# Optimization experiments

Hardware: AMD Instinct MI355X
Metric: run time of the kernel (lower is better)

## Reference

```python
import jax, jax.numpy as jnp
import numpy as np

EPS = 1e-6
NUM_HEADS = 16

def _favor_positive_features(x):
    # softmax-style normalized positive features along last dim
    p = jnp.exp(x - jnp.max(x, axis=-1, keepdims=True))
    return p / (jnp.sum(p, axis=-1, keepdims=True) + EPS)

def setup_inputs() -> dict:
    key = jax.random.key(0)
    ks = jax.random.split(key, 9)
    B, L, D = 2, 2048, 1024
    s = 0.02
    return {
        "hidden_states": jax.random.normal(ks[0], (B, L, D), dtype=jnp.float32),
        # Linear weights stored as [in, out] (y = x @ W + b), matching torch Linear math
        "Wq": jax.random.normal(ks[1], (D, D), dtype=jnp.float32) * s,
        "bq": jnp.zeros((D,), dtype=jnp.float32),
        "Wk": jax.random.normal(ks[2], (D, D), dtype=jnp.float32) * s,
        "bk": jnp.zeros((D,), dtype=jnp.float32),
        "Wv": jax.random.normal(ks[3], (D, D), dtype=jnp.float32) * s,
        "bv": jnp.zeros((D,), dtype=jnp.float32),
        "Wo": jax.random.normal(ks[4], (D, D), dtype=jnp.float32) * s,
        "bo": jnp.zeros((D,), dtype=jnp.float32),
    }

def reference(hidden_states, Wq, bq, Wk, bk, Wv, bv, Wo, bo):
    B, L, D = hidden_states.shape
    H = NUM_HEADS
    hd = D // H

    def split_heads(x):  # [B,L,D] -> [B,H,L,hd]
        return x.reshape(B, L, H, hd).transpose(0, 2, 1, 3)

    q = split_heads(hidden_states @ Wq + bq)
    k = split_heads(hidden_states @ Wk + bk)
    v = split_heads(hidden_states @ Wv + bv)

    q = _favor_positive_features(q)
    k = _favor_positive_features(k)

    # quadratic scores as in the original module
    numerator = jnp.einsum('bhld,bhmd->bhlm', q, k)
    # einsum(q, ones) over d == sum_d q, broadcast over m (identical math)
    denominator = jnp.sum(q, axis=-1, keepdims=True)  # [B,H,L,1]
    attention_probs = numerator / (denominator + EPS)
    # dropout prob = 0.0 -> identity
    context = jnp.einsum('bhlm,bhmd->bhld', attention_probs, v)
    context = context.transpose(0, 2, 1, 3).reshape(B, L, D)
    return context @ Wo + bo
```

## Files before the change

kernel.cpp:

```cpp
#include <hip/hip_runtime.h>


#define EPSV 1e-6f
#define MDIM 4096
#define DDIM 1024
#define HEADS 16
#define HD 64

typedef __attribute__((ext_vector_type(8))) _Float16 half8;
typedef __attribute__((ext_vector_type(4))) _Float16 half4;
typedef __attribute__((ext_vector_type(4))) float f32x4;

__device__ inline void gld_lds16(const _Float16* g, _Float16* l) {
    __builtin_amdgcn_global_load_lds(
        (const __attribute__((address_space(1))) unsigned int*)g,
        (__attribute__((address_space(3))) unsigned int*)l, 16, 0, 0);
}

__global__ __launch_bounds__(256) void xhalf_kernel(const float* __restrict__ x,
                                                    _Float16* __restrict__ xh)
{
    const int i = (blockIdx.x * 256 + threadIdx.x) * 8;
    const float4 v0 = *(const float4*)&x[i];
    const float4 v1 = *(const float4*)&x[i + 4];
    half8 h;
    h[0] = (_Float16)v0.x; h[1] = (_Float16)v0.y; h[2] = (_Float16)v0.z; h[3] = (_Float16)v0.w;
    h[4] = (_Float16)v1.x; h[5] = (_Float16)v1.y; h[6] = (_Float16)v1.z; h[7] = (_Float16)v1.w;
    *(half8*)&xh[i] = h;
}

__global__ __launch_bounds__(256) void wsplit_kernel(
    const float* __restrict__ W0, const float* __restrict__ W1,
    const float* __restrict__ W2, const float* __restrict__ W3,
    _Float16* __restrict__ T0h, _Float16* __restrict__ T0l,
    _Float16* __restrict__ T1h, _Float16* __restrict__ T1l,
    _Float16* __restrict__ T2h, _Float16* __restrict__ T2l,
    _Float16* __restrict__ T3h, _Float16* __restrict__ T3l)
{
    const float* W; _Float16* Th; _Float16* Tl;
    if (blockIdx.z == 0)      { W = W0; Th = T0h; Tl = T0l; }
    else if (blockIdx.z == 1) { W = W1; Th = T1h; Tl = T1l; }
    else if (blockIdx.z == 2) { W = W2; Th = T2h; Tl = T2l; }
    else                      { W = W3; Th = T3h; Tl = T3l; }

    __shared__ float t[32][33];
    const int tt = threadIdx.x;
    const int r = tt >> 3, c4 = (tt & 7) * 4;
    const int k0 = blockIdx.x * 32, n0 = blockIdx.y * 32;

    const float4 v = *(const float4*)&W[(size_t)(k0 + r) * DDIM + n0 + c4];
    t[r][c4 + 0] = v.x; t[r][c4 + 1] = v.y; t[r][c4 + 2] = v.z; t[r][c4 + 3] = v.w;
    __syncthreads();

    const float x0 = t[c4 + 0][r], x1 = t[c4 + 1][r], x2 = t[c4 + 2][r], x3 = t[c4 + 3][r];
    half4 h, l;
    h[0] = (_Float16)x0; l[0] = (_Float16)((x0 - (float)h[0]) * 256.0f);
    h[1] = (_Float16)x1; l[1] = (_Float16)((x1 - (float)h[1]) * 256.0f);
    h[2] = (_Float16)x2; l[2] = (_Float16)((x2 - (float)h[2]) * 256.0f);
    h[3] = (_Float16)x3; l[3] = (_Float16)((x3 - (float)h[3]) * 256.0f);
    *(half4*)&Th[(size_t)(n0 + r) * DDIM + k0 + c4] = h;
    *(half4*)&Tl[(size_t)(n0 + r) * DDIM + k0 + c4] = l;
}

template<int WJ>
__global__ __launch_bounds__(256, 2) void gemm_mfma(
    const _Float16* __restrict__ A,
    const _Float16* __restrict__ B0h, const _Float16* __restrict__ B0l,
    const _Float16* __restrict__ B1h, const _Float16* __restrict__ B1l,
    const _Float16* __restrict__ B2h, const _Float16* __restrict__ B2l,
    const float* __restrict__ bias0, const float* __restrict__ bias1, const float* __restrict__ bias2,
    float* __restrict__ C0, float* __restrict__ C1, float* __restrict__ C2)
{
    const _Float16* Bh; const _Float16* Bl; const float* bias; float* C;
    if (blockIdx.z == 0)      { Bh = B0h; Bl = B0l; bias = bias0; C = C0; }
    else if (blockIdx.z == 1) { Bh = B1h; Bl = B1l; bias = bias1; C = C1; }
    else                      { Bh = B2h; Bl = B2l; bias = bias2; C = C2; }

    constexpr int FA = 8;
    constexpr int FB = 2 * WJ;
    constexpr int NF = FA + 2 * FB;
    constexpr int FPW = NF / 4;
    constexpr int NT = DDIM / 32;

    __shared__ __align__(16) _Float16 lds[2][NF * 512];

    const int tid = threadIdx.x;
    const int w = tid >> 6, l = tid & 63;
    const int row0 = blockIdx.x * 128, col0 = blockIdx.y * (32 * WJ);
    const int wr = w >> 1, wc = w & 1;

    const int lrow = (l & 15);
    const int lk   = (l >> 4) * 8;

    const _Float16* gsrc[FPW];
    #pragma unroll
    for (int u = 0; u < FPW; ++u) {
        const int g = w * FPW + u;
        const _Float16* src; int outer;
        if (g < FA)           { src = A;  outer = row0 + g * 16; }
        else if (g < FA + FB) { src = Bh; outer = col0 + (g - FA) * 16; }
        else                  { src = Bl; outer = col0 + (g - FA - FB) * 16; }
        gsrc[u] = src + (size_t)(outer + lrow) * DDIM + lk;
    }

    f32x4 acc1[4][WJ], acc2[4][WJ];
    #pragma unroll
    for (int i = 0; i < 4; ++i)
        #pragma unroll
        for (int j = 0; j < WJ; ++j) {
            acc1[i][j] = (f32x4){0.f, 0.f, 0.f, 0.f};
            acc2[i][j] = (f32x4){0.f, 0.f, 0.f, 0.f};
        }

    #pragma unroll
    for (int u = 0; u < FPW; ++u)
        gld_lds16(gsrc[u], &lds[0][(w * FPW + u) * 512]);
    __syncthreads();

    int cur = 0;
    for (int t = 0; t < NT; ++t) {
        if (t + 1 < NT) {
            const int kc = (t + 1) * 32;
            #pragma unroll
            for (int u = 0; u < FPW; ++u)
                gld_lds16(gsrc[u] + kc, &lds[cur ^ 1][(w * FPW + u) * 512]);
        }

        const _Float16* lbase = &lds[cur][0];
        half8 a[4], bh[WJ], bl[WJ];
        #pragma unroll
        for (int i = 0; i < 4; ++i)
            a[i] = *(const half8*)&lbase[(wr * 4 + i) * 512 + l * 8];
        #pragma unroll
        for (int j = 0; j < WJ; ++j) {
            bh[j] = *(const half8*)&lbase[(FA + wc * WJ + j) * 512 + l * 8];
            bl[j] = *(const half8*)&lbase[(FA + FB + wc * WJ + j) * 512 + l * 8];
        }
        #pragma unroll
        for (int i = 0; i < 4; ++i)
            #pragma unroll
            for (int j = 0; j < WJ; ++j) {
                acc1[i][j] = __builtin_amdgcn_mfma_f32_16x16x32_f16(a[i], bh[j], acc1[i][j], 0, 0, 0);
                acc2[i][j] = __builtin_amdgcn_mfma_f32_16x16x32_f16(a[i], bl[j], acc2[i][j], 0, 0, 0);
            }

        __syncthreads();
        cur ^= 1;
    }

    #pragma unroll
    for (int j = 0; j < WJ; ++j) {
        const int col = col0 + (wc * WJ + j) * 16 + lrow;
        const float bb = bias[col];
        #pragma unroll
        for (int i = 0; i < 4; ++i) {
            const int rbase = row0 + (wr * 4 + i) * 16 + (l >> 4) * 4;
            #pragma unroll
            for (int q = 0; q < 4; ++q)
                C[(size_t)(rbase + q) * DDIM + col] =
                    acc1[i][j][q] + acc2[i][j][q] * 0.00390625f + bb;
        }
    }
}

__global__ __launch_bounds__(256) void feature_kernel(float* __restrict__ buf,
                                                      float* __restrict__ den)
{
    const int wid  = blockIdx.x * 4 + (threadIdx.x >> 6);
    const int lane = threadIdx.x & 63;
    const int row = wid >> 4;
    const int h   = wid & 15;
    float* p = buf + (size_t)row * DDIM + h * HD;

    const float v = p[lane];
    float m = v;
    #pragma unroll
    for (int o = 32; o; o >>= 1) m = fmaxf(m, __shfl_xor(m, o, 64));
    const float e = expf(v - m);
    float s = e;
    #pragma unroll
    for (int o = 32; o; o >>= 1) s += __shfl_xor(s, o, 64);
    const float q = e / (s + EPSV);
    p[lane] = q;
    if (den != nullptr) {
        float d = q;
        #pragma unroll
        for (int o = 32; o; o >>= 1) d += __shfl_xor(d, o, 64);
        if (lane == 0) den[wid] = d;
    }
}

#define MSUB 32
__global__ __launch_bounds__(256) void kv_partial_kernel(
    const float* __restrict__ Kf, const float* __restrict__ V, float* __restrict__ KVp)
{
    const int z = blockIdx.x;
    const int chunk = z & 7;
    const int bh = z >> 3;
    const int h = bh & 15;
    const int b = bh >> 4;

    __shared__ float Ks[MSUB][HD];
    __shared__ float Vs[MSUB][HD];

    const int t = threadIdx.x;
    const int d0 = (t >> 4) * 4;
    const int e0 = (t & 15) * 4;
    float acc[4][4];
    #pragma unroll
    for (int i = 0; i < 4; ++i)
        #pragma unroll
        for (int j = 0; j < 4; ++j) acc[i][j] = 0.f;

    const int base_tok = b * 2048 + chunk * 256;
    for (int sc = 0; sc < 8; ++sc) {
        __syncthreads();
        #pragma unroll
        for (int u = 0; u < 2; ++u) {
            const int f = t + u * 256;
            const int tok = f >> 4;
            const int c4 = (f & 15) * 4;
            const size_t g = (size_t)(base_tok + sc * MSUB + tok) * DDIM + h * HD + c4;
            *(float4*)&Ks[tok][c4] = *(const float4*)&Kf[g];
            *(float4*)&Vs[tok][c4] = *(const float4*)&V[g];
        }
        __syncthreads();
        #pragma unroll
        for (int mm = 0; mm < MSUB; ++mm) {
            const float4 k4 = *(const float4*)&Ks[mm][d0];
            const float4 v4 = *(const float4*)&Vs[mm][e0];
            const float kr[4] = {k4.x, k4.y, k4.z, k4.w};
            const float vr[4] = {v4.x, v4.y, v4.z, v4.w};
            #pragma unroll
            for (int i = 0; i < 4; ++i)
                #pragma unroll
                for (int j = 0; j < 4; ++j)
                    acc[i][j] = fmaf(kr[i], vr[j], acc[i][j]);
        }
    }
    float* outp = KVp + (size_t)z * 4096;
    #pragma unroll
    for (int i = 0; i < 4; ++i)
        *(float4*)&outp[(d0 + i) * HD + e0] =
            make_float4(acc[i][0], acc[i][1], acc[i][2], acc[i][3]);
}

__global__ __launch_bounds__(256) void kv_reduce_kernel(const float* __restrict__ KVp,
                                                        float* __restrict__ KV)
{
    const int idx = blockIdx.x * 256 + threadIdx.x;
    const int bh = idx >> 12;
    const int off = idx & 4095;
    float s = 0.f;
    #pragma unroll
    for (int c = 0; c < 8; ++c) s += KVp[(size_t)(bh * 8 + c) * 4096 + off];
    KV[idx] = s;
}

__global__ __launch_bounds__(256) void context_kernel(
    const float* __restrict__ QF, const float* __restrict__ KV, const float* __restrict__ den,
    _Float16* __restrict__ Ch)
{
    const int z = blockIdx.x;
    const int tc = z & 31;
    const int bh = z >> 5;
    const int h = bh & 15;
    const int b = bh >> 4;

    __shared__ float KVs[HD][HD];
    const int t = threadIdx.x;
    #pragma unroll
    for (int u = 0; u < 4; ++u) {
        const int f = t + u * 256;
        *(float4*)&KVs[0][f * 4] = *(const float4*)&KV[(size_t)bh * 4096 + f * 4];
    }
    __syncthreads();

    const int wave = t >> 6;
    const int lane = t & 63;
    for (int it = 0; it < 16; ++it) {
        const int tok = tc * 64 + it * 4 + wave;
        const int row = b * 2048 + tok;
        const size_t idx = (size_t)row * DDIM + h * HD + lane;
        const float qv = QF[idx];
        float acc = 0.f;
        #pragma unroll
        for (int e = 0; e < 64; ++e) {
            const float qe = __shfl(qv, e, 64);
            acc = fmaf(qe, KVs[e][lane], acc);
        }
        const float r = acc / (den[row * HEADS + h] + EPSV);
        Ch[idx] = (_Float16)r;
    }
}

extern "C" void kernel_launch(void* const* d_in, const int* in_sizes, int n_in,
                              void* d_out, int out_size, void* d_ws, size_t ws_size,
                              hipStream_t stream)
{
    const float* X  = (const float*)d_in[0];
    const float* Wq = (const float*)d_in[1];
    const float* bq = (const float*)d_in[2];
    const float* Wk = (const float*)d_in[3];
    const float* bk = (const float*)d_in[4];
    const float* Wv = (const float*)d_in[5];
    const float* bv = (const float*)d_in[6];
    const float* Wo = (const float*)d_in[7];
    const float* bo = (const float*)d_in[8];
    float* out = (float*)d_out;

    float* ws  = (float*)d_ws;
    float* Q   = ws;
    float* Kb  = ws + 4194304;
    float* Vb  = ws + 8388608;
    float* den = ws + 12582912;
    float* KV  = den + 65536;
    float* KVp = KV + 131072;
    _Float16* Xh  = (_Float16*)(KVp + 1048576);
    _Float16* Wqh = Xh + 4194304;
    _Float16* Wql = Wqh + 1048576;
    _Float16* Wkh = Wql + 1048576;
    _Float16* Wkl = Wkh + 1048576;
    _Float16* Wvh = Wkl + 1048576;
    _Float16* Wvl = Wvh + 1048576;
    _Float16* Woh = Wvl + 1048576;
    _Float16* Wol = Woh + 1048576;
    _Float16* Ch  = Xh;

    xhalf_kernel<<<2048, 256, 0, stream>>>(X, Xh);
    wsplit_kernel<<<dim3(32, 32, 4), 256, 0, stream>>>(
        Wq, Wk, Wv, Wo, Wqh, Wql, Wkh, Wkl, Wvh, Wvl, Woh, Wol);

    gemm_mfma<4><<<dim3(32, 8, 3), 256, 0, stream>>>(
        Xh, Wqh, Wql, Wkh, Wkl, Wvh, Wvl, bq, bk, bv, Q, Kb, Vb);

    feature_kernel<<<16384, 256, 0, stream>>>(Q, den);
    feature_kernel<<<16384, 256, 0, stream>>>(Kb, nullptr);

    kv_partial_kernel<<<256, 256, 0, stream>>>(Kb, Vb, KVp);
    kv_reduce_kernel<<<512, 256, 0, stream>>>(KVp, KV);

    context_kernel<<<1024, 256, 0, stream>>>(Q, KV, den, Ch);

    gemm_mfma<2><<<dim3(32, 16, 1), 256, 0, stream>>>(
        Ch, Woh, Wol, Woh, Wol, Woh, Wol, bo, bo, bo, out, out, out);
}
```

Baseline: 304.2 us.

## Load B weight fragments directly from global into registers, stage only A in LDS

The GEMM now stages only the A tile in LDS through async global-to-LDS loads, while each wave reads its own B high/low fragments straight from global memory into registers every k-step. This shrinks LDS use per block and drops the LDS round trip for B, which may allow more occupancy. In exchange, B loads are synchronous, un-prefetched global loads issued right before the MFMAs, so their latency is exposed. B tiles are also re-read by both wave rows instead of being shared through LDS.

New measurement: 395.5 us. 30.0% more time.

```diff
diff --git a/kernel.cpp b/kernel.cpp
--- a/kernel.cpp
+++ b/kernel.cpp
@@ -77,12 +77,9 @@
     else                      { Bh = B2h; Bl = B2l; bias = bias2; C = C2; }
 
     constexpr int FA = 8;
-    constexpr int FB = 2 * WJ;
-    constexpr int NF = FA + 2 * FB;
-    constexpr int FPW = NF / 4;
     constexpr int NT = DDIM / 32;
 
-    __shared__ __align__(16) _Float16 lds[2][NF * 512];
+    __shared__ __align__(16) _Float16 lds[2][FA * 512];
 
     const int tid = threadIdx.x;
     const int w = tid >> 6, l = tid & 63;
@@ -92,15 +89,20 @@
     const int lrow = (l & 15);
     const int lk   = (l >> 4) * 8;
 
-    const _Float16* gsrc[FPW];
-    #pragma unroll
-    for (int u = 0; u < FPW; ++u) {
-        const int g = w * FPW + u;
-        const _Float16* src; int outer;
-        if (g < FA)           { src = A;  outer = row0 + g * 16; }
-        else if (g < FA + FB) { src = Bh; outer = col0 + (g - FA) * 16; }
-        else                  { src = Bl; outer = col0 + (g - FA - FB) * 16; }
-        gsrc[u] = src + (size_t)(outer + lrow) * DDIM + lk;
+    const _Float16* gsrcA[2];
+    #pragma unroll
+    for (int u = 0; u < 2; ++u) {
+        const int g = w * 2 + u;
+        gsrcA[u] = A + (size_t)(row0 + g * 16 + lrow) * DDIM + lk;
+    }
+
+    const _Float16* bhp[WJ];
+    const _Float16* blp[WJ];
+    #pragma unroll
+    for (int j = 0; j < WJ; ++j) {
+        const int bcol = col0 + (wc * WJ + j) * 16 + lrow;
+        bhp[j] = Bh + (size_t)bcol * DDIM + lk;
+        blp[j] = Bl + (size_t)bcol * DDIM + lk;
     }
 
     f32x4 acc1[4][WJ], acc2[4][WJ];
@@ -113,35 +115,37 @@
         }
 
     #pragma unroll
-    for (int u = 0; u < FPW; ++u)
-        gld_lds16(gsrc[u], &lds[0][(w * FPW + u) * 512]);
+    for (int u = 0; u < 2; ++u)
+        gld_lds16(gsrcA[u], &lds[0][(w * 2 + u) * 512]);
     __syncthreads();
 
     int cur = 0;
     for (int t = 0; t < NT; ++t) {
+        const int kc = t * 32;
+
+        half8 bhr[WJ], blr[WJ];
+        #pragma unroll
+        for (int j = 0; j < WJ; ++j) bhr[j] = *(const half8*)(bhp[j] + kc);
+        #pragma unroll
+        for (int j = 0; j < WJ; ++j) blr[j] = *(const half8*)(blp[j] + kc);
+
         if (t + 1 < NT) {
-            const int kc = (t + 1) * 32;
             #pragma unroll
-            for (int u = 0; u < FPW; ++u)
-                gld_lds16(gsrc[u] + kc, &lds[cur ^ 1][(w * FPW + u) * 512]);
-        }
-
-        const _Float16* lbase = &lds[cur][0];
-        half8 a[4], bh[WJ], bl[WJ];
+            for (int u = 0; u < 2; ++u)
+                gld_lds16(gsrcA[u] + kc + 32, &lds[cur ^ 1][(w * 2 + u) * 512]);
+        }
+
+        half8 a[4];
         #pragma unroll
         for (int i = 0; i < 4; ++i)
-            a[i] = *(const half8*)&lbase[(wr * 4 + i) * 512 + l * 8];
-        #pragma unroll
-        for (int j = 0; j < WJ; ++j) {
-            bh[j] = *(const half8*)&lbase[(FA + wc * WJ + j) * 512 + l * 8];
-            bl[j] = *(const half8*)&lbase[(FA + FB + wc * WJ + j) * 512 + l * 8];
-        }
+            a[i] = *(const half8*)&lds[cur][(wr * 4 + i) * 512 + l * 8];
+
         #pragma unroll
         for (int i = 0; i < 4; ++i)
             #pragma unroll
             for (int j = 0; j < WJ; ++j) {
-                acc1[i][j] = __builtin_amdgcn_mfma_f32_16x16x32_f16(a[i], bh[j], acc1[i][j], 0, 0, 0);
-                acc2[i][j] = __builtin_amdgcn_mfma_f32_16x16x32_f16(a[i], bl[j], acc2[i][j], 0, 0, 0);
+                acc1[i][j] = __builtin_amdgcn_mfma_f32_16x16x32_f16(a[i], bhr[j], acc1[i][j], 0, 0, 0);
+                acc2[i][j] = __builtin_amdgcn_mfma_f32_16x16x32_f16(a[i], blr[j], acc2[i][j], 0, 0, 0);
             }
 
         __syncthreads();
```
